# Kernel optimization log

Hardware: AMD Instinct MI355X
Metric: run time of the kernel (lower is better)

## Reference

```python
import jax, jax.numpy as jnp
import numpy as np

B, S, D, E, N = 2, 1024, 1024, 64, 16  # batch, seq, model_dim, embedding_dim, num_splats


def setup_inputs() -> dict:
    key = jax.random.key(0)
    ks = jax.random.split(key, 8)
    inv_sqrt_d = 1.0 / np.sqrt(D)
    return {
        "token_embeddings": jax.random.normal(ks[0], (B, S, D), jnp.float32),
        # position encoder Linear(D, E)
        "pos_W": jax.random.normal(ks[1], (D, E), jnp.float32) * inv_sqrt_d,
        "pos_b": jnp.zeros((E,), jnp.float32),
        "positional_bias": jax.random.normal(ks[2], (1024, E), jnp.float32) * 0.01,
        "splat_positions": jax.random.normal(ks[3], (N, E), jnp.float32) * 0.2,
        "splat_log_scales": jnp.zeros((N,), jnp.float32),
        # q/k/v Linear(D, D, bias=False)
        "q_W": jax.random.normal(ks[4], (D, D), jnp.float32) * inv_sqrt_d,
        "k_W": jax.random.normal(ks[5], (D, D), jnp.float32) * inv_sqrt_d,
        "v_W": jax.random.normal(ks[6], (D, D), jnp.float32) * inv_sqrt_d,
        "splat_gates": jnp.full((N,), 0.5, jnp.float32),
        "residual_weight": jnp.asarray(0.8, jnp.float32),
        "ln_w": jnp.ones((D,), jnp.float32),
        "ln_b": jnp.zeros((D,), jnp.float32),
    }


def reference(token_embeddings, pos_W, pos_b, positional_bias, splat_positions,
              splat_log_scales, q_W, k_W, v_W, splat_gates, residual_weight,
              ln_w, ln_b):
    b, s, d = token_embeddings.shape
    # token positions in splat embedding space: tanh(Linear(x)) + pos_bias[:S]
    positions = jnp.tanh(token_embeddings @ pos_W + pos_b) + positional_bias[:s][None]  # [B,S,E]
    # spatial influence per splat: Gaussian of distance, clamped scales, floor 0.01
    diff = positions[:, :, None, :] - splat_positions[None, None]  # [B,S,N,E]
    dist_sq = jnp.sum(diff * diff, axis=-1)                         # [B,S,N]
    scales = jnp.clip(jnp.exp(splat_log_scales), 0.3, 2.0)
    influence = jnp.maximum(jnp.exp(-0.5 * dist_sq / (scales * scales)), 0.01)  # [B,S,N]

    q = token_embeddings @ q_W
    k = token_embeddings @ k_W
    v = token_embeddings @ v_W

    w = jnp.transpose(influence, (2, 0, 1))      # [N,B,S]
    qw = q[None] * w[..., None]                  # [N,B,S,D]
    kw = k[None] * w[..., None]
    scores = jnp.einsum('nbid,nbjd->nbij', qw, kw) / jnp.sqrt(jnp.asarray(d, jnp.float32))
    causal = jnp.tril(jnp.ones((s, s), bool))
    scores = jnp.where(causal[None, None], scores, -1e9)
    attn = jax.nn.softmax(scores, axis=-1)       # [N,B,S,S]
    out = jnp.einsum('nbij,bjd->nbid', attn, v)  # [N,B,S,D]

    gates = jax.nn.sigmoid(splat_gates)[:, None, None, None]
    combined = jnp.mean(out * gates, axis=0)     # [B,S,D]

    rw = jax.nn.sigmoid(residual_weight)
    o = rw * token_embeddings + (1.0 - rw) * combined
    # LayerNorm (eps=1e-5)
    mu = jnp.mean(o, axis=-1, keepdims=True)
    var = jnp.mean((o - mu) ** 2, axis=-1, keepdims=True)
    return (o - mu) / jnp.sqrt(var + 1e-5) * ln_w + ln_b
```

## Files before the change

### kernel.cpp

```cpp
#include <hip/hip_runtime.h>
#include <hip/hip_bf16.h>
#include <hip/hip_fp16.h>

using bf16 = __hip_bfloat16;
typedef __attribute__((ext_vector_type(8))) short short8;
typedef __attribute__((ext_vector_type(4))) float f32x4;

static constexpr int Bb = 2, Ss = 1024, Dd = 1024, Ee = 64, Nn = 16;

struct Params {
    const float *X, *posW, *posB, *pbias, *spos, *lsc, *qW, *kW, *vW, *gates, *rwp, *lnw, *lnb;
    bf16 *Xb, *Wt, *WpT, *QKV, *Vt, *Aav;
    __half *wh;
    float *qk0, *qk1, *cb0, *cb1, *out;
};

__device__ __forceinline__ unsigned short f2bfr(float f) {
    __hip_bfloat16 h = __float2bfloat16(f);
    return *reinterpret_cast<unsigned short*>(&h);
}

#define GL_LDS(gp, lp) __builtin_amdgcn_global_load_lds( \
    (const __attribute__((address_space(1))) void*)(gp), \
    (__attribute__((address_space(3))) void*)(lp), 16, 0, 0)

__device__ __forceinline__ void do_transpose_f2b(
    const float* __restrict__ in, bf16* __restrict__ out,
    int R, int C, int bx, int by, char* sm)
{
    float (*tile)[65] = (float(*)[65])sm;
    int tx = threadIdx.x & 63, ty = threadIdx.x >> 6;
    int r0 = by * 64, c0 = bx * 64;
    #pragma unroll
    for (int i = 0; i < 16; ++i)
        tile[ty + i*4][tx] = in[(long)(r0 + ty + i*4)*C + c0 + tx];
    __syncthreads();
    #pragma unroll
    for (int i = 0; i < 16; ++i)
        out[(long)(c0 + ty + i*4)*R + r0 + tx] = __float2bfloat16(tile[tx][ty + i*4]);
    __syncthreads();
}

__device__ __forceinline__ void do_transpose_bf(
    const bf16* __restrict__ in, bf16* __restrict__ out,
    int R, int C, int bx, int by, char* sm)
{
    bf16 (*tile)[65] = (bf16(*)[65])sm;
    int tx = threadIdx.x & 63, ty = threadIdx.x >> 6;
    int r0 = by * 64, c0 = bx * 64;
    #pragma unroll
    for (int i = 0; i < 16; ++i)
        tile[ty + i*4][tx] = in[(long)(r0 + ty + i*4)*C + c0 + tx];
    __syncthreads();
    #pragma unroll
    for (int i = 0; i < 16; ++i)
        out[(long)(c0 + ty + i*4)*R + r0 + tx] = tile[tx][ty + i*4];
    __syncthreads();
}

template<int OUT_BF16>
__device__ __forceinline__ void do_gemm64(
    const bf16* __restrict__ Ab, const bf16* __restrict__ Bw, void* __restrict__ Cv,
    int Nc, int m0, int n0, int kBeg, int kEnd, float scale, char* sm)
{
    short* lA = (short*)sm;
    short* lB = (short*)(sm + 4096);
    int tid = threadIdx.x, wid = tid >> 6, lane = tid & 63;
    int wn = wid * 32, r16 = lane & 15, quad = lane >> 4;

    f32x4 acc[4][2];
    #pragma unroll
    for (int i = 0; i < 4; ++i)
        #pragma unroll
        for (int j = 0; j < 2; ++j)
            #pragma unroll
            for (int c = 0; c < 4; ++c) acc[i][j][c] = 0.f;

    int ra  = tid >> 2, ka  = (tid & 3) * 8;
    int c1  = tid + 256, rb1 = c1 >> 2, kb1 = (c1 & 3) * 8;
    const short* Ag = (const short*)Ab;
    const short* Bg = (const short*)Bw;

    for (int k0 = kBeg; k0 < kEnd; k0 += 32) {
        __syncthreads();
        GL_LDS(Ag + (long)(m0+ra)*1024 + k0 + ka,  lA + tid*8);
        GL_LDS(Bg + (long)(n0+ra)*1024 + k0 + ka,  lB + tid*8);
        GL_LDS(Bg + (long)(n0+rb1)*1024 + k0 + kb1, lB + c1*8);
        __syncthreads();

        short8 af[4], bfv[2];
        #pragma unroll
        for (int i = 0; i < 4; ++i) af[i]  = *(const short8*)(lA + (i*16 + r16)*32 + quad*8);
        #pragma unroll
        for (int j = 0; j < 2; ++j) bfv[j] = *(const short8*)(lB + (wn + j*16 + r16)*32 + quad*8);
        #pragma unroll
        for (int i = 0; i < 4; ++i)
            #pragma unroll
            for (int j = 0; j < 2; ++j)
                acc[i][j] = __builtin_amdgcn_mfma_f32_16x16x32_bf16(af[i], bfv[j], acc[i][j], 0, 0, 0);
    }

    if (OUT_BF16) {
        bf16* C = (bf16*)Cv;
        #pragma unroll
        for (int i = 0; i < 4; ++i)
            #pragma unroll
            for (int j = 0; j < 2; ++j)
                #pragma unroll
                for (int rr = 0; rr < 4; ++rr)
                    C[(long)(m0 + i*16 + quad*4 + rr)*Nc + n0 + wn + j*16 + r16] =
                        __float2bfloat16(acc[i][j][rr] * scale);
    } else {
        float* C = (float*)Cv;
        #pragma unroll
        for (int i = 0; i < 4; ++i)
            #pragma unroll
            for (int j = 0; j < 2; ++j)
                #pragma unroll
                for (int rr = 0; rr < 4; ++rr)
                    C[(long)(m0 + i*16 + quad*4 + rr)*Nc + n0 + wn + j*16 + r16] =
                        acc[i][j][rr] * scale;
    }
}

__device__ __forceinline__ void do_pos(const Params& p, int m0, char* sm)
{
    short* lA = (short*)sm;
    short* lB = (short*)(sm + 4096);
    float (*P)[65]  = (float(*)[65])(sm + 8192);
    float (*sp)[65] = (float(*)[65])(sm + 8192 + 64*65*4);

    int tid = threadIdx.x, wid = tid >> 6, lane = tid & 63;
    int r16 = lane & 15, quad = lane >> 4;

    for (int idx = tid; idx < 16*64; idx += 256)
        sp[idx >> 6][idx & 63] = p.spos[idx];

    f32x4 acc[4];
    #pragma unroll
    for (int j = 0; j < 4; ++j)
        #pragma unroll
        for (int c = 0; c < 4; ++c) acc[j][c] = 0.f;

    int ra = tid >> 2, ka = (tid & 3) * 8;
    const short* Ag = (const short*)p.Xb;
    const short* Bg = (const short*)p.WpT;

    for (int k0 = 0; k0 < Dd; k0 += 32) {
        __syncthreads();
        GL_LDS(Ag + (long)(m0+ra)*1024 + k0 + ka, lA + tid*8);
        GL_LDS(Bg + (long)ra*1024 + k0 + ka,      lB + tid*8);
        __syncthreads();

        short8 af = *(const short8*)(lA + (wid*16 + r16)*32 + quad*8);
        #pragma unroll
        for (int j = 0; j < 4; ++j) {
            short8 bfv = *(const short8*)(lB + (j*16 + r16)*32 + quad*8);
            acc[j] = __builtin_amdgcn_mfma_f32_16x16x32_bf16(af, bfv, acc[j], 0, 0, 0);
        }
    }

    #pragma unroll
    for (int j = 0; j < 4; ++j)
        #pragma unroll
        for (int rr = 0; rr < 4; ++rr) {
            int rl  = wid*16 + quad*4 + rr;
            int col = j*16 + r16;
            int srow = (m0 + rl) & (Ss - 1);
            P[rl][col] = tanhf(acc[j][rr] + p.posB[col]) + p.pbias[srow*Ee + col];
        }
    __syncthreads();

    int n  = tid & 15;
    int rb = (tid >> 4) * 4;
    float sc = __expf(p.lsc[n]);
    sc = fminf(fmaxf(sc, 0.3f), 2.0f);
    float inv2 = -0.5f / (sc * sc);
    #pragma unroll
    for (int rr = 0; rr < 4; ++rr) {
        int row = rb + rr;
        float d2 = 0.f;
        #pragma unroll 16
        for (int e = 0; e < 64; ++e) {
            float df = P[row][e] - sp[n][e];
            d2 += df * df;
        }
        float infl = fmaxf(__expf(d2 * inv2), 0.01f);
        p.wh[(long)(m0 + row)*Nn + n] = __float2half(infl);
    }
}

__global__ __launch_bounds__(256) void k_prep(Params p)
{
    __shared__ __align__(16) char sm[64*65*4];
    int z = blockIdx.z;
    if (z < 3) {
        const float* w = (z == 0) ? p.qW : (z == 1) ? p.kW : p.vW;
        do_transpose_f2b(w, p.Wt + (long)z*Dd*Dd, Dd, Dd, blockIdx.x, blockIdx.y, sm);
    } else if (blockIdx.x == 0) {
        do_transpose_f2b(p.posW, p.WpT, Dd, Ee, 0, blockIdx.y, sm);
    } else {
        int job = blockIdx.y * 15 + (blockIdx.x - 1);
        const float4* src = (const float4*)p.X;
        ushort4* dst = (ushort4*)p.Xb;
        for (int idx = job*256 + (int)threadIdx.x; idx < Bb*Ss*Dd/4; idx += 240*256) {
            float4 v = src[idx];
            ushort4 y;
            y.x = f2bfr(v.x); y.y = f2bfr(v.y); y.z = f2bfr(v.z); y.w = f2bfr(v.w);
            dst[idx] = y;
        }
    }
}

__global__ __launch_bounds__(256) void k_qkv_pos(Params p)
{
    __shared__ __align__(16) char sm[8192 + 64*65*4 + 16*65*4];
    int job = blockIdx.x;
    if (job < 768) {
        int z = job >> 8, t = job & 255;
        int bm = t >> 3, bn = t & 7;
        do_gemm64<1>(p.Xb, p.Wt + (long)z*Dd*Dd, p.QKV + (long)z*2048*1024,
                     Dd, bm*64, bn*128, 0, Dd, 1.f, sm);
    } else {
        do_pos(p, (job - 768)*64, sm);
    }
}

__global__ __launch_bounds__(256) void k_qkt_vt(Params p)
{
    __shared__ __align__(16) char sm[12288];
    int job = blockIdx.x;
    if (job < 288) {
        int pairIdx = job >> 1, h = job & 1;
        int b = pairIdx / 72, t = pairIdx % 72;
        int acc = 0, bm = 0, bn = 0;
        #pragma unroll
        for (int u = 0; u < 16; ++u) {
            int c = (u >> 1) + 1;
            if (t < acc + c) { bm = u; bn = t - acc; break; }
            acc += c;
        }
        const bf16* Qb = p.QKV + (long)b*Ss*Dd;
        const bf16* Kb = p.QKV + (long)2048*1024 + (long)b*Ss*Dd;
        float* dst = (h ? p.qk1 : p.qk0) + (long)b*Ss*Ss;
        do_gemm64<0>(Qb, Kb, dst, Ss, bm*64, bn*128, h*512, h*512 + 512, 0.03125f, sm);
    } else {
        int j2 = job - 288;
        int b = j2 >> 7, tt = j2 & 127;
        int r = tt >> 3, cp = (tt & 7) * 2;
        const bf16* Vb = p.QKV + (long)2*2048*1024 + (long)b*Ss*Dd;
        bf16* Vtb = p.Vt + (long)b*Dd*Ss;
        do_transpose_bf(Vb, Vtb, Ss, Dd, cp,     r, sm);
        do_transpose_bf(Vb, Vtb, Ss, Dd, cp + 1, r, sm);
    }
}

__global__ __launch_bounds__(256) void k_softmax(Params p)
{
    __shared__ __align__(16) char sm[36864 + 256];
    __half2 (*wt)[9] = (__half2(*)[9])sm;
    float (*wi4)[16] = (float(*)[16])(sm + 36864);

    int base = blockIdx.x * 4, b = blockIdx.y;
    int tid = threadIdx.x, wid = tid >> 6, lane = tid & 63;
    int imax = base + 3;

    const __half*  whb  = p.wh + (long)b*Ss*Nn;
    const __half2* whb2 = (const __half2*)whb;

    for (int j = tid; j <= imax; j += 256) {
        #pragma unroll
        for (int h = 0; h < 8; ++h)
            wt[j][h] = whb2[j*8 + h];
    }
    if (tid < 64) wi4[tid >> 4][tid & 15] =
        __half2float(whb[(long)(base + (tid >> 4))*16 + (tid & 15)]);
    __syncthreads();

    int i = base + wid;
    const float* q0 = p.qk0 + ((long)b*Ss + i)*Ss;
    const float* q1 = p.qk1 + ((long)b*Ss + i)*Ss;
    bf16* arow      = p.Aav + ((long)b*Ss + i)*Ss;

    float wiR[16], m[16], l[16];
    #pragma unroll
    for (int n = 0; n < 16; ++n) { wiR[n] = wi4[wid][n]; m[n] = -1e30f; l[n] = 0.f; }

    for (int j = lane; j <= i; j += 64) {
        float q = q0[j] + q1[j];
        #pragma unroll
        for (int h = 0; h < 8; ++h) {
            float2 f = __half22float2(wt[j][h]);
            m[2*h]     = fmaxf(m[2*h],     wiR[2*h]     * f.x * q);
            m[2*h + 1] = fmaxf(m[2*h + 1], wiR[2*h + 1] * f.y * q);
        }
    }
    #pragma unroll
    for (int n = 0; n < 16; ++n)
        #pragma unroll
        for (int off = 32; off > 0; off >>= 1)
            m[n] = fmaxf(m[n], __shfl_xor(m[n], off));

    for (int j = lane; j <= i; j += 64) {
        float q = q0[j] + q1[j];
        #pragma unroll
        for (int h = 0; h < 8; ++h) {
            float2 f = __half22float2(wt[j][h]);
            l[2*h]     += __expf(wiR[2*h]     * f.x * q - m[2*h]);
            l[2*h + 1] += __expf(wiR[2*h + 1] * f.y * q - m[2*h + 1]);
        }
    }
    #pragma unroll
    for (int n = 0; n < 16; ++n)
        #pragma unroll
        for (int off = 32; off > 0; off >>= 1)
            l[n] += __shfl_xor(l[n], off);

    float coef[16];
    #pragma unroll
    for (int n = 0; n < 16; ++n) {
        float g  = p.gates[n];
        float sg = 1.f / (1.f + __expf(-g));
        coef[n]  = sg / (16.f * l[n]);
    }

    for (int j = lane; j < Ss; j += 64) {
        float a = 0.f;
        if (j <= i) {
            float q = q0[j] + q1[j];
            #pragma unroll
            for (int h = 0; h < 8; ++h) {
                float2 f = __half22float2(wt[j][h]);
                a += coef[2*h]     * __expf(wiR[2*h]     * f.x * q - m[2*h]);
                a += coef[2*h + 1] * __expf(wiR[2*h + 1] * f.y * q - m[2*h + 1]);
            }
        }
        arow[j] = __float2bfloat16(a);
    }
}

__global__ __launch_bounds__(256) void k_av(Params p)
{
    __shared__ __align__(16) char sm[12288];
    int job = blockIdx.x;
    int b, bm, bn, kBeg, kEnd;
    if (job < 256) {
        b = job >> 7; int t = job & 127; bm = t >> 3; bn = t & 7;
        kBeg = 0; kEnd = bm*64 + 64; if (kEnd > 512) kEnd = 512;
    } else {
        int j = job - 256;
        b = j >> 6; int t = j & 63; bm = 8 + (t >> 3); bn = t & 7;
        kBeg = 512; kEnd = bm*64 + 64;
    }
    const bf16* Ab = p.Aav + (long)b*Ss*Ss;
    const bf16* Bw = p.Vt + (long)b*Dd*Ss;
    float* dst = (job < 256 ? p.cb0 : p.cb1) + (long)b*Ss*Dd;
    do_gemm64<0>(Ab, Bw, dst, Dd, bm*64, bn*128, kBeg, kEnd, 1.f, sm);
}

__global__ __launch_bounds__(256) void k_epilogue(Params p)
{
    __shared__ float rs[4], rq[4];
    long row = blockIdx.x;
    int tid = threadIdx.x, wid = tid >> 6, lane = tid & 63;
    float rw = 1.f / (1.f + __expf(-p.rwp[0]));

    float4 c0 = ((const float4*)(p.cb0 + row*Dd))[tid];
    int s = (int)(row & (Ss - 1));
    float4 c1 = make_float4(0.f, 0.f, 0.f, 0.f);
    if (s >= 512) c1 = ((const float4*)(p.cb1 + row*Dd))[tid];
    float4 xv = ((const float4*)(p.X + row*Dd))[tid];

    float o[4];
    o[0] = rw * xv.x + (1.f - rw) * (c0.x + c1.x);
    o[1] = rw * xv.y + (1.f - rw) * (c0.y + c1.y);
    o[2] = rw * xv.z + (1.f - rw) * (c0.z + c1.z);
    o[3] = rw * xv.w + (1.f - rw) * (c0.w + c1.w);

    float sm1 = o[0] + o[1] + o[2] + o[3];
    float sq  = o[0]*o[0] + o[1]*o[1] + o[2]*o[2] + o[3]*o[3];
    #pragma unroll
    for (int off = 32; off > 0; off >>= 1) { sm1 += __shfl_xor(sm1, off); sq += __shfl_xor(sq, off); }
    if (lane == 0) { rs[wid] = sm1; rq[wid] = sq; }
    __syncthreads();
    sm1 = rs[0] + rs[1] + rs[2] + rs[3];
    sq  = rq[0] + rq[1] + rq[2] + rq[3];
    float mu  = sm1 * (1.f/1024.f);
    float var = sq * (1.f/1024.f) - mu*mu;
    float inv = rsqrtf(var + 1e-5f);

    float4 lw = ((const float4*)p.lnw)[tid];
    float4 lb = ((const float4*)p.lnb)[tid];
    float4 y;
    y.x = (o[0] - mu)*inv*lw.x + lb.x;
    y.y = (o[1] - mu)*inv*lw.y + lb.y;
    y.z = (o[2] - mu)*inv*lw.z + lb.z;
    y.w = (o[3] - mu)*inv*lw.w + lb.w;
    ((float4*)(p.out + row*Dd))[tid] = y;
}

extern "C" void kernel_launch(void* const* d_in, const int* in_sizes, int n_in,
                              void* d_out, int out_size, void* d_ws, size_t ws_size,
                              hipStream_t stream)
{
    Params prm;
    prm.X     = (const float*)d_in[0];
    prm.posW  = (const float*)d_in[1];
    prm.posB  = (const float*)d_in[2];
    prm.pbias = (const float*)d_in[3];
    prm.spos  = (const float*)d_in[4];
    prm.lsc   = (const float*)d_in[5];
    prm.qW    = (const float*)d_in[6];
    prm.kW    = (const float*)d_in[7];
    prm.vW    = (const float*)d_in[8];
    prm.gates = (const float*)d_in[9];
    prm.rwp   = (const float*)d_in[10];
    prm.lnw   = (const float*)d_in[11];
    prm.lnb   = (const float*)d_in[12];

    char* ws = (char*)d_ws;
    size_t off = 0;
    prm.Xb  = (bf16*)(ws + off);   off += (size_t)Bb*Ss*Dd*2;
    prm.Wt  = (bf16*)(ws + off);   off += (size_t)3*Dd*Dd*2;
    prm.WpT = (bf16*)(ws + off);   off += (size_t)Ee*Dd*2;
    prm.QKV = (bf16*)(ws + off);   off += (size_t)3*Bb*Ss*Dd*2;
    prm.Vt  = (bf16*)(ws + off);   off += (size_t)Bb*Dd*Ss*2;
    prm.Aav = (bf16*)(ws + off);   off += (size_t)Bb*Ss*Ss*2;
    prm.wh  = (__half*)(ws + off); off += (size_t)Bb*Ss*Nn*2;
    prm.qk0 = (float*)(ws + off);  off += (size_t)Bb*Ss*Ss*4;
    prm.qk1 = (float*)(ws + off);  off += (size_t)Bb*Ss*Ss*4;
    prm.cb0 = (float*)(ws + off);  off += (size_t)Bb*Ss*Dd*4;
    prm.cb1 = (float*)(ws + off);  off += (size_t)Bb*Ss*Dd*4;
    prm.out = (float*)d_out;
    (void)ws_size;

    k_prep    <<<dim3(16,16,4), 256, 0, stream>>>(prm);
    k_qkv_pos <<<800,            256, 0, stream>>>(prm);
    k_qkt_vt  <<<544,            256, 0, stream>>>(prm);
    k_softmax <<<dim3(256, 2),   256, 0, stream>>>(prm);
    k_av      <<<384,            256, 0, stream>>>(prm);
    k_epilogue<<<2048,           256, 0, stream>>>(prm);
}
```

Before: 180.0 us.

## Double GEMM K-tile to 64 and XOR-swizzle LDS layout

The shared bf16 MFMA GEMM helper now stages 64-wide K slices per iteration instead of 32, so each tile needs half as many loop iterations and barrier pairs. LDS chunks are stored with an XOR swizzle of the 16-byte column group by row, and the fragment reads apply the same swizzle, to reduce bank conflicts in the MFMA operand loads. The LDS footprint doubles to 24 KB in the QK^T and AV kernels, which may lower occupancy.

```diff
diff --git a/kernel.cpp b/kernel.cpp
--- a/kernel.cpp
+++ b/kernel.cpp
@@ -64,7 +64,7 @@
     int Nc, int m0, int n0, int kBeg, int kEnd, float scale, char* sm)
 {
     short* lA = (short*)sm;
-    short* lB = (short*)(sm + 4096);
+    short* lB = (short*)(sm + 8192);
     int tid = threadIdx.x, wid = tid >> 6, lane = tid & 63;
     int wn = wid * 32, r16 = lane & 15, quad = lane >> 4;
 
@@ -76,28 +76,49 @@
             #pragma unroll
             for (int c = 0; c < 4; ++c) acc[i][j][c] = 0.f;
 
-    int ra  = tid >> 2, ka  = (tid & 3) * 8;
-    int c1  = tid + 256, rb1 = c1 >> 2, kb1 = (c1 & 3) * 8;
     const short* Ag = (const short*)Ab;
     const short* Bg = (const short*)Bw;
 
-    for (int k0 = kBeg; k0 < kEnd; k0 += 32) {
+    int arow[2], akg[2], brow[4], bkg[4];
+    #pragma unroll
+    for (int j = 0; j < 2; ++j) {
+        int c = tid + j*256; arow[j] = c >> 3; akg[j] = (c & 7) ^ (arow[j] & 7);
+    }
+    #pragma unroll
+    for (int j = 0; j < 4; ++j) {
+        int c = tid + j*256; brow[j] = c >> 3; bkg[j] = (c & 7) ^ (brow[j] & 7);
+    }
+
+    for (int k0 = kBeg; k0 < kEnd; k0 += 64) {
         __syncthreads();
-        GL_LDS(Ag + (long)(m0+ra)*1024 + k0 + ka,  lA + tid*8);
-        GL_LDS(Bg + (long)(n0+ra)*1024 + k0 + ka,  lB + tid*8);
-        GL_LDS(Bg + (long)(n0+rb1)*1024 + k0 + kb1, lB + c1*8);
+        #pragma unroll
+        for (int j = 0; j < 2; ++j)
+            GL_LDS(Ag + (long)(m0 + arow[j])*1024 + k0 + akg[j]*8, lA + (tid + j*256)*8);
+        #pragma unroll
+        for (int j = 0; j < 4; ++j)
+            GL_LDS(Bg + (long)(n0 + brow[j])*1024 + k0 + bkg[j]*8, lB + (tid + j*256)*8);
         __syncthreads();
 
-        short8 af[4], bfv[2];
-        #pragma unroll
-        for (int i = 0; i < 4; ++i) af[i]  = *(const short8*)(lA + (i*16 + r16)*32 + quad*8);
-        #pragma unroll
-        for (int j = 0; j < 2; ++j) bfv[j] = *(const short8*)(lB + (wn + j*16 + r16)*32 + quad*8);
-        #pragma unroll
-        for (int i = 0; i < 4; ++i)
-            #pragma unroll
-            for (int j = 0; j < 2; ++j)
-                acc[i][j] = __builtin_amdgcn_mfma_f32_16x16x32_bf16(af[i], bfv[j], acc[i][j], 0, 0, 0);
+        #pragma unroll
+        for (int kk = 0; kk < 2; ++kk) {
+            int kc = kk*4 + quad;
+            short8 af[4], bfv[2];
+            #pragma unroll
+            for (int i = 0; i < 4; ++i) {
+                int r = i*16 + r16;
+                af[i] = *(const short8*)(lA + r*64 + (kc ^ (r & 7))*8);
+            }
+            #pragma unroll
+            for (int j = 0; j < 2; ++j) {
+                int r = wn + j*16 + r16;
+                bfv[j] = *(const short8*)(lB + r*64 + (kc ^ (r & 7))*8);
+            }
+            #pragma unroll
+            for (int i = 0; i < 4; ++i)
+                #pragma unroll
+                for (int j = 0; j < 2; ++j)
+                    acc[i][j] = __builtin_amdgcn_mfma_f32_16x16x32_bf16(af[i], bfv[j], acc[i][j], 0, 0, 0);
+        }
     }
 
     if (OUT_BF16) {
@@ -228,7 +249,7 @@
 
 __global__ __launch_bounds__(256) void k_qkt_vt(Params p)
 {
-    __shared__ __align__(16) char sm[12288];
+    __shared__ __align__(16) char sm[24576];
     int job = blockIdx.x;
     if (job < 288) {
         int pairIdx = job >> 1, h = job & 1;
@@ -341,7 +362,7 @@
 
 __global__ __launch_bounds__(256) void k_av(Params p)
 {
-    __shared__ __align__(16) char sm[12288];
+    __shared__ __align__(16) char sm[24576];
     int job = blockIdx.x;
     int b, bm, bn, kBeg, kEnd;
     if (job < 256) {
```

Result: faster. 172.7 us (-4.1%).

## Double-buffer GEMM LDS tiles with XOR swizzle, remap QKV blocks per XCD

Applied to the files above, without the earlier changes.

Rewrites the shared 64x128 bf16 GEMM helper to keep two LDS buffers, so the next k-slice is loaded while MFMAs run on the current one. It also XOR-swizzles the k-chunk placement to cut LDS bank conflicts. The QKV projection launch gets a block-to-tile mapping that groups tiles sharing the same weight panel onto one XCD, and the positional/influence job moves into the QK^T kernel. The change raises LDS use per block, which may lower occupancy, and relies on only one barrier per iteration plus the async global-to-LDS load ordering being correct.

```diff
diff --git a/kernel.cpp b/kernel.cpp
--- a/kernel.cpp
+++ b/kernel.cpp
@@ -63,8 +63,10 @@
     const bf16* __restrict__ Ab, const bf16* __restrict__ Bw, void* __restrict__ Cv,
     int Nc, int m0, int n0, int kBeg, int kEnd, float scale, char* sm)
 {
-    short* lA = (short*)sm;
-    short* lB = (short*)(sm + 4096);
+    short* lA0 = (short*)sm;
+    short* lA1 = (short*)(sm + 4096);
+    short* lB0 = (short*)(sm + 8192);
+    short* lB1 = (short*)(sm + 16384);
     int tid = threadIdx.x, wid = tid >> 6, lane = tid & 63;
     int wn = wid * 32, r16 = lane & 15, quad = lane >> 4;
 
@@ -76,28 +78,47 @@
             #pragma unroll
             for (int c = 0; c < 4; ++c) acc[i][j][c] = 0.f;
 
-    int ra  = tid >> 2, ka  = (tid & 3) * 8;
-    int c1  = tid + 256, rb1 = c1 >> 2, kb1 = (c1 & 3) * 8;
     const short* Ag = (const short*)Ab;
     const short* Bg = (const short*)Bw;
 
-    for (int k0 = kBeg; k0 < kEnd; k0 += 32) {
-        __syncthreads();
-        GL_LDS(Ag + (long)(m0+ra)*1024 + k0 + ka,  lA + tid*8);
-        GL_LDS(Bg + (long)(n0+ra)*1024 + k0 + ka,  lB + tid*8);
-        GL_LDS(Bg + (long)(n0+rb1)*1024 + k0 + kb1, lB + c1*8);
-        __syncthreads();
-
+    int ar  = tid >> 2,            akc  = (tid & 3) ^ ((ar  >> 1) & 3);
+    int br0 = tid >> 2,            bkc0 = (tid & 3) ^ ((br0 >> 1) & 3);
+    int cB1 = tid + 256;
+    int br1 = cB1 >> 2,            bkc1 = (cB1 & 3) ^ ((br1 >> 1) & 3);
+
+    auto stage = [&](short* lA, short* lB, int k0) {
+        GL_LDS(Ag + (long)(m0 + ar )*1024 + k0 + akc *8, lA + tid*8);
+        GL_LDS(Bg + (long)(n0 + br0)*1024 + k0 + bkc0*8, lB + tid*8);
+        GL_LDS(Bg + (long)(n0 + br1)*1024 + k0 + bkc1*8, lB + cB1*8);
+    };
+    auto compute = [&](short* lA, short* lB) {
         short8 af[4], bfv[2];
         #pragma unroll
-        for (int i = 0; i < 4; ++i) af[i]  = *(const short8*)(lA + (i*16 + r16)*32 + quad*8);
-        #pragma unroll
-        for (int j = 0; j < 2; ++j) bfv[j] = *(const short8*)(lB + (wn + j*16 + r16)*32 + quad*8);
+        for (int i = 0; i < 4; ++i) {
+            int r = i*16 + r16;
+            af[i] = *(const short8*)(lA + r*32 + (quad ^ ((r >> 1) & 3))*8);
+        }
+        #pragma unroll
+        for (int j = 0; j < 2; ++j) {
+            int r = wn + j*16 + r16;
+            bfv[j] = *(const short8*)(lB + r*32 + (quad ^ ((r >> 1) & 3))*8);
+        }
         #pragma unroll
         for (int i = 0; i < 4; ++i)
             #pragma unroll
             for (int j = 0; j < 2; ++j)
                 acc[i][j] = __builtin_amdgcn_mfma_f32_16x16x32_bf16(af[i], bfv[j], acc[i][j], 0, 0, 0);
+    };
+
+    short *cA = lA0, *cB = lB0, *nA = lA1, *nB = lB1;
+    stage(cA, cB, kBeg);
+    for (int k0 = kBeg; k0 < kEnd; k0 += 32) {
+        __syncthreads();
+        if (k0 + 32 < kEnd) stage(nA, nB, k0 + 32);
+        compute(cA, cB);
+        short* t;
+        t = cA; cA = nA; nA = t;
+        t = cB; cB = nB; nB = t;
     }
 
     if (OUT_BF16) {
@@ -212,23 +233,21 @@
     }
 }
 
-__global__ __launch_bounds__(256) void k_qkv_pos(Params p)
-{
-    __shared__ __align__(16) char sm[8192 + 64*65*4 + 16*65*4];
-    int job = blockIdx.x;
-    if (job < 768) {
-        int z = job >> 8, t = job & 255;
-        int bm = t >> 3, bn = t & 7;
-        do_gemm64<1>(p.Xb, p.Wt + (long)z*Dd*Dd, p.QKV + (long)z*2048*1024,
-                     Dd, bm*64, bn*128, 0, Dd, 1.f, sm);
-    } else {
-        do_pos(p, (job - 768)*64, sm);
-    }
+__global__ __launch_bounds__(256) void k_qkv(Params p)
+{
+    __shared__ __align__(16) char sm[24576];
+    int idx = blockIdx.x;
+    int xcd = idx & 7, s = idx >> 3;
+    int combo = xcd * 3 + (s >> 5);
+    int z = combo >> 3, bn = combo & 7;
+    int bm = s & 31;
+    do_gemm64<1>(p.Xb, p.Wt + (long)z*Dd*Dd, p.QKV + (long)z*2048*1024,
+                 Dd, bm*64, bn*128, 0, Dd, 1.f, sm);
 }
 
 __global__ __launch_bounds__(256) void k_qkt_vt(Params p)
 {
-    __shared__ __align__(16) char sm[12288];
+    __shared__ __align__(16) char sm[28992];
     int job = blockIdx.x;
     if (job < 288) {
         int pairIdx = job >> 1, h = job & 1;
@@ -244,7 +263,7 @@
         const bf16* Kb = p.QKV + (long)2048*1024 + (long)b*Ss*Dd;
         float* dst = (h ? p.qk1 : p.qk0) + (long)b*Ss*Ss;
         do_gemm64<0>(Qb, Kb, dst, Ss, bm*64, bn*128, h*512, h*512 + 512, 0.03125f, sm);
-    } else {
+    } else if (job < 544) {
         int j2 = job - 288;
         int b = j2 >> 7, tt = j2 & 127;
         int r = tt >> 3, cp = (tt & 7) * 2;
@@ -252,6 +271,8 @@
         bf16* Vtb = p.Vt + (long)b*Dd*Ss;
         do_transpose_bf(Vb, Vtb, Ss, Dd, cp,     r, sm);
         do_transpose_bf(Vb, Vtb, Ss, Dd, cp + 1, r, sm);
+    } else {
+        do_pos(p, (job - 544)*64, sm);
     }
 }
 
@@ -341,7 +362,7 @@
 
 __global__ __launch_bounds__(256) void k_av(Params p)
 {
-    __shared__ __align__(16) char sm[12288];
+    __shared__ __align__(16) char sm[24576];
     int job = blockIdx.x;
     int b, bm, bn, kBeg, kEnd;
     if (job < 256) {
@@ -435,8 +456,8 @@
     (void)ws_size;
 
     k_prep    <<<dim3(16,16,4), 256, 0, stream>>>(prm);
-    k_qkv_pos <<<800,            256, 0, stream>>>(prm);
-    k_qkt_vt  <<<544,            256, 0, stream>>>(prm);
+    k_qkv     <<<768,            256, 0, stream>>>(prm);
+    k_qkt_vt  <<<576,            256, 0, stream>>>(prm);
     k_softmax <<<dim3(256, 2),   256, 0, stream>>>(prm);
     k_av      <<<384,            256, 0, stream>>>(prm);
     k_epilogue<<<2048,           256, 0, stream>>>(prm);
```

Result: no change. 180.4 us (+0.2%).
